# Kernel optimization log

Measured on AMD Instinct MI355X. Metric: run time of the kernel, lower is better.

## Reference

```python
import jax, jax.numpy as jnp
import numpy as np


def setup_inputs() -> dict:
    key = jax.random.key(0)
    k1, k2 = jax.random.split(key)
    B, H, W, D, K = 32, 64, 64, 64, 512
    x = jax.random.normal(k1, (B, H, W, D), dtype=jnp.float32)
    w = jax.random.normal(k2, (D, K), dtype=jnp.float32) * 0.05  # codebook (embedding_dim, num_embeddings)
    return {"x": x, "w": w}


def reference(x, w):
    commitment_cost = 1.0
    D = w.shape[0]
    z_e = x
    flat = x.reshape(-1, D)  # [N, D]
    # squared euclidean distances to each code: ||f||^2 - 2 f.w + ||w||^2 -> [N, K]
    distances = (jnp.sum(flat * flat, axis=1, keepdims=True)
                 - 2.0 * flat @ w
                 + jnp.sum(w * w, axis=0, keepdims=True))
    encoding_indices = jnp.argmax(-distances, axis=1).reshape(x.shape[:-1])  # [B,H,W]
    z_q = w.T[encoding_indices]  # embedding lookup -> [B,H,W,D]
    e_latent_loss = jnp.mean((jax.lax.stop_gradient(z_q) - z_e) ** 2)
    q_latent_loss = jnp.mean((z_q - jax.lax.stop_gradient(z_e)) ** 2)
    latent_loss = q_latent_loss + commitment_cost * e_latent_loss
    z_q_st = z_e + jax.lax.stop_gradient(z_q - z_e)  # straight-through estimator
    return encoding_indices, z_q_st, z_e, latent_loss
```

## Files before the change

kernel.cpp:

```cpp
#include <hip/hip_runtime.h>
#include <hip/hip_bf16.h>

#define NROWS   131072
#define DDIM    64
#define KCODES  512

#define RPB     128
#define NBLK    (NROWS / RPB)
#define CAP     16
#define THRESH  0.04f

#define WS_PART 0
#define WS_WT   2048
#define WS_WSQ  34816
#define WS_WTH  35328
#define WS_WTL  51712
#define WS_END  68096
#define WS_NEED_MFMA ((size_t)WS_END * sizeof(float))
#define WS_NEED_FALL ((size_t)35328 * sizeof(float))

#define NBLK_FB 1024

typedef __attribute__((ext_vector_type(8))) short short8;
typedef __attribute__((ext_vector_type(4))) float f32x4;

static __device__ __forceinline__ unsigned short f2bf(float v) {
  union { __hip_bfloat16 b; unsigned short u; } cv;
  cv.b = __float2bfloat16(v);
  return cv.u;
}
static __device__ __forceinline__ float bf2f(unsigned short u) {
  union { float f; unsigned v; } r;
  r.v = ((unsigned)u) << 16;
  return r.f;
}

static __device__ __forceinline__ float dot64(const float* __restrict__ xr,
                                              const float* __restrict__ wk) {
  const float4* __restrict__ w4 = (const float4*)wk;
  const float4* __restrict__ x4 = (const float4*)xr;
  float d = 0.f;
  {
    float4 wa0 = w4[0], wa1 = w4[1], wa2 = w4[2], wa3 = w4[3];
    float4 wa4 = w4[4], wa5 = w4[5], wa6 = w4[6], wa7 = w4[7];
    float4 xa0 = x4[0], xa1 = x4[1], xa2 = x4[2], xa3 = x4[3];
    float4 xa4 = x4[4], xa5 = x4[5], xa6 = x4[6], xa7 = x4[7];
    d = __builtin_fmaf(xa0.x, wa0.x, d); d = __builtin_fmaf(xa0.y, wa0.y, d);
    d = __builtin_fmaf(xa0.z, wa0.z, d); d = __builtin_fmaf(xa0.w, wa0.w, d);
    d = __builtin_fmaf(xa1.x, wa1.x, d); d = __builtin_fmaf(xa1.y, wa1.y, d);
    d = __builtin_fmaf(xa1.z, wa1.z, d); d = __builtin_fmaf(xa1.w, wa1.w, d);
    d = __builtin_fmaf(xa2.x, wa2.x, d); d = __builtin_fmaf(xa2.y, wa2.y, d);
    d = __builtin_fmaf(xa2.z, wa2.z, d); d = __builtin_fmaf(xa2.w, wa2.w, d);
    d = __builtin_fmaf(xa3.x, wa3.x, d); d = __builtin_fmaf(xa3.y, wa3.y, d);
    d = __builtin_fmaf(xa3.z, wa3.z, d); d = __builtin_fmaf(xa3.w, wa3.w, d);
    d = __builtin_fmaf(xa4.x, wa4.x, d); d = __builtin_fmaf(xa4.y, wa4.y, d);
    d = __builtin_fmaf(xa4.z, wa4.z, d); d = __builtin_fmaf(xa4.w, wa4.w, d);
    d = __builtin_fmaf(xa5.x, wa5.x, d); d = __builtin_fmaf(xa5.y, wa5.y, d);
    d = __builtin_fmaf(xa5.z, wa5.z, d); d = __builtin_fmaf(xa5.w, wa5.w, d);
    d = __builtin_fmaf(xa6.x, wa6.x, d); d = __builtin_fmaf(xa6.y, wa6.y, d);
    d = __builtin_fmaf(xa6.z, wa6.z, d); d = __builtin_fmaf(xa6.w, wa6.w, d);
    d = __builtin_fmaf(xa7.x, wa7.x, d); d = __builtin_fmaf(xa7.y, wa7.y, d);
    d = __builtin_fmaf(xa7.z, wa7.z, d); d = __builtin_fmaf(xa7.w, wa7.w, d);
  }
  {
    float4 wb0 = w4[8],  wb1 = w4[9],  wb2 = w4[10], wb3 = w4[11];
    float4 wb4 = w4[12], wb5 = w4[13], wb6 = w4[14], wb7 = w4[15];
    float4 xb0 = x4[8],  xb1 = x4[9],  xb2 = x4[10], xb3 = x4[11];
    float4 xb4 = x4[12], xb5 = x4[13], xb6 = x4[14], xb7 = x4[15];
    d = __builtin_fmaf(xb0.x, wb0.x, d); d = __builtin_fmaf(xb0.y, wb0.y, d);
    d = __builtin_fmaf(xb0.z, wb0.z, d); d = __builtin_fmaf(xb0.w, wb0.w, d);
    d = __builtin_fmaf(xb1.x, wb1.x, d); d = __builtin_fmaf(xb1.y, wb1.y, d);
    d = __builtin_fmaf(xb1.z, wb1.z, d); d = __builtin_fmaf(xb1.w, wb1.w, d);
    d = __builtin_fmaf(xb2.x, wb2.x, d); d = __builtin_fmaf(xb2.y, wb2.y, d);
    d = __builtin_fmaf(xb2.z, wb2.z, d); d = __builtin_fmaf(xb2.w, wb2.w, d);
    d = __builtin_fmaf(xb3.x, wb3.x, d); d = __builtin_fmaf(xb3.y, wb3.y, d);
    d = __builtin_fmaf(xb3.z, wb3.z, d); d = __builtin_fmaf(xb3.w, wb3.w, d);
    d = __builtin_fmaf(xb4.x, wb4.x, d); d = __builtin_fmaf(xb4.y, wb4.y, d);
    d = __builtin_fmaf(xb4.z, wb4.z, d); d = __builtin_fmaf(xb4.w, wb4.w, d);
    d = __builtin_fmaf(xb5.x, wb5.x, d); d = __builtin_fmaf(xb5.y, wb5.y, d);
    d = __builtin_fmaf(xb5.z, wb5.z, d); d = __builtin_fmaf(xb5.w, wb5.w, d);
    d = __builtin_fmaf(xb6.x, wb6.x, d); d = __builtin_fmaf(xb6.y, wb6.y, d);
    d = __builtin_fmaf(xb6.z, wb6.z, d); d = __builtin_fmaf(xb6.w, wb6.w, d);
    d = __builtin_fmaf(xb7.x, wb7.x, d); d = __builtin_fmaf(xb7.y, wb7.y, d);
    d = __builtin_fmaf(xb7.z, wb7.z, d); d = __builtin_fmaf(xb7.w, wb7.w, d);
  }
  return d;
}

__global__ void vq_prep_base(const float* __restrict__ w, float* __restrict__ wT,
                             float* __restrict__ wsq) {
  int g = blockIdx.x * 256 + threadIdx.x;
  wT[g] = w[(g & 63) * KCODES + (g >> 6)];
  if (g < KCODES) {
    float s = __fmul_rn(w[g], w[g]);
    for (int dd = 1; dd < DDIM; ++dd) {
      float v = w[dd * KCODES + g];
      s = __fadd_rn(s, __fmul_rn(v, v));
    }
    wsq[g] = s;
  }
}

__global__ void vq_prep_bf16(const float* __restrict__ wT,
                             unsigned short* __restrict__ wTh,
                             unsigned short* __restrict__ wTl) {
  int g = blockIdx.x * 256 + threadIdx.x;
  float v = wT[g];
  unsigned short h = f2bf(v);
  wTh[g] = h;
  wTl[g] = f2bf(v - bf2f(h));
}

__global__ __launch_bounds__(256) void vq_mfma(
    const float* __restrict__ x, const float* __restrict__ wT,
    const float* __restrict__ wsq, const unsigned short* __restrict__ wTh,
    const unsigned short* __restrict__ wTl, float* __restrict__ out_idx,
    float* __restrict__ out_zq, float* __restrict__ out_ze,
    float* __restrict__ lossPart) {
  __shared__ float xf[RPB * 68];
  __shared__ __attribute__((aligned(16))) char Bb[2][16384];
  __shared__ float wsq_s[KCODES];
  __shared__ float sumf_s[RPB];
  __shared__ int   idx_s[RPB];
  __shared__ int   cnt[RPB];
  __shared__ int   cand[RPB][CAP];
  __shared__ float loss_s[4];

  const int tid = threadIdx.x;
  const int wv = tid >> 6;
  const int lane = tid & 63;
  const int lr = lane & 15;
  const int kg = lane >> 4;
  const int rowBase = blockIdx.x * RPB;
  const float* xb = x + (size_t)rowBase * DDIM;

#pragma unroll
  for (int j = 0; j < 8; ++j) {
    int off = j * 1024 + tid * 4;
    float4 v = *(const float4*)(xb + off);
    int row = off >> 6, d0 = off & 63;
    *(float4*)&xf[row * 68 + d0] = v;
  }
  if (tid < 128) {
    cnt[tid] = 0;
    *(float4*)&wsq_s[tid * 4] = *(const float4*)&wsq[tid * 4];
  }

  const char* gH = (const char*)wTh;
  const char* gL = (const char*)wTl;
  float4 rH0, rH1, rL0, rL1;
#define LOADT(t)                                                   \
  {                                                                \
    const char* bh = gH + (size_t)(t) * 8192;                      \
    const char* bl = gL + (size_t)(t) * 8192;                      \
    rH0 = *(const float4*)(bh + tid * 16);                         \
    rH1 = *(const float4*)(bh + 4096 + tid * 16);                  \
    rL0 = *(const float4*)(bl + tid * 16);                         \
    rL1 = *(const float4*)(bl + 4096 + tid * 16);                  \
  }
  const int p0 = tid * 16, p1 = 4096 + tid * 16;
  const int cc0 = p0 >> 7, cc1 = p1 >> 7;
  const int w0 = cc0 * 128 + ((p0 & 127) ^ ((cc0 & 7) << 4));
  const int w1 = cc1 * 128 + ((p1 & 127) ^ ((cc1 & 7) << 4));
#define WRITET(buf)                                                \
  {                                                                \
    *(float4*)(Bb[buf] + w0) = rH0;                                \
    *(float4*)(Bb[buf] + w1) = rH1;                                \
    *(float4*)(Bb[buf] + 8192 + w0) = rL0;                         \
    *(float4*)(Bb[buf] + 8192 + w1) = rL1;                         \
  }

  LOADT(0);
  __syncthreads();

  short8 ah[2][2], al[2][2];
#pragma unroll
  for (int m = 0; m < 2; ++m)
#pragma unroll
    for (int kb = 0; kb < 2; ++kb) {
      const float* src = &xf[(wv * 32 + m * 16 + lr) * 68 + kb * 32 + kg * 8];
      short8 h, l;
#pragma unroll
      for (int j = 0; j < 8; ++j) {
        float v = src[j];
        unsigned short hu = f2bf(v);
        h[j] = (short)hu;
        l[j] = (short)f2bf(v - bf2f(hu));
      }
      ah[m][kb] = h;
      al[m][kb] = l;
    }

  if (lane < 32) {
    const float* xr = &xf[(wv * 32 + lane) * 68];
    float rr[8];
#pragma unroll
    for (int j = 0; j < 8; ++j) rr[j] = __fmul_rn(xr[j], xr[j]);
#pragma unroll
    for (int b = 1; b < 8; ++b)
#pragma unroll
      for (int j = 0; j < 8; ++j)
        rr[j] = __fadd_rn(rr[j], __fmul_rn(xr[b * 8 + j], xr[b * 8 + j]));
    float s01 = __fadd_rn(rr[0], rr[1]), s23 = __fadd_rn(rr[2], rr[3]);
    float s45 = __fadd_rn(rr[4], rr[5]), s67 = __fadd_rn(rr[6], rr[7]);
    sumf_s[wv * 32 + lane] = __fadd_rn(__fadd_rn(s01, s23), __fadd_rn(s45, s67));
  }

  WRITET(0);
  LOADT(1);
  __syncthreads();

  float rmin[2][4];
#pragma unroll
  for (int m = 0; m < 2; ++m)
#pragma unroll
    for (int q = 0; q < 4; ++q) rmin[m][q] = 3.4e38f;

  for (int t = 0; t < 8; ++t) {
    const char* bufc = Bb[t & 1];
    float sc[2][4][4];
#pragma unroll
    for (int n = 0; n < 4; ++n) {
      const int cc = n * 16 + lr;
      const int rowb = cc * 128;
      const int srow = (cc & 7) << 4;
      short8 bh0 = *(const short8*)(bufc + rowb + ((kg * 16) ^ srow));
      short8 bh1 = *(const short8*)(bufc + rowb + ((64 + kg * 16) ^ srow));
      short8 bl0 = *(const short8*)(bufc + 8192 + rowb + ((kg * 16) ^ srow));
      short8 bl1 = *(const short8*)(bufc + 8192 + rowb + ((64 + kg * 16) ^ srow));
      float wsqk = wsq_s[t * 64 + cc];
#pragma unroll
      for (int m = 0; m < 2; ++m) {
        f32x4 acc = {0.f, 0.f, 0.f, 0.f};
        acc = __builtin_amdgcn_mfma_f32_16x16x32_bf16(ah[m][0], bh0, acc, 0, 0, 0);
        acc = __builtin_amdgcn_mfma_f32_16x16x32_bf16(al[m][0], bh0, acc, 0, 0, 0);
        acc = __builtin_amdgcn_mfma_f32_16x16x32_bf16(ah[m][0], bl0, acc, 0, 0, 0);
        acc = __builtin_amdgcn_mfma_f32_16x16x32_bf16(ah[m][1], bh1, acc, 0, 0, 0);
        acc = __builtin_amdgcn_mfma_f32_16x16x32_bf16(al[m][1], bh1, acc, 0, 0, 0);
        acc = __builtin_amdgcn_mfma_f32_16x16x32_bf16(ah[m][1], bl1, acc, 0, 0, 0);
#pragma unroll
        for (int q = 0; q < 4; ++q)
          sc[m][n][q] = __builtin_fmaf(-2.0f, acc[q], wsqk);
      }
    }
#pragma unroll
    for (int m = 0; m < 2; ++m)
#pragma unroll
      for (int q = 0; q < 4; ++q) {
        float tm = fminf(fminf(sc[m][0][q], sc[m][1][q]),
                         fminf(sc[m][2][q], sc[m][3][q]));
#pragma unroll
        for (int s = 1; s < 16; s <<= 1) tm = fminf(tm, __shfl_xor(tm, s));
        float rm = fminf(rmin[m][q], tm);
        rmin[m][q] = rm;
        float thr = rm + THRESH;
        int rl = wv * 32 + m * 16 + kg * 4 + q;
#pragma unroll
        for (int n = 0; n < 4; ++n) {
          if (sc[m][n][q] <= thr) {
            int slot = atomicAdd(&cnt[rl], 1);
            if (slot < CAP) cand[rl][slot] = t * 64 + n * 16 + lr;
          }
        }
      }
    __syncthreads();
    if (t < 7) {
      WRITET((t + 1) & 1);
      if (t < 6) LOADT(t + 2);
      __syncthreads();
    }
  }

#pragma unroll 1
  for (int half = 0; half < 2; ++half) {
    const int myrow = wv * 32 + half * 16 + (lane >> 2);
    const int sub = lane & 3;
    const int cnr = cnt[myrow];
    const float* xr = &xf[myrow * 68];
    const float sf = sumf_s[myrow];
    float bd = 3.4e38f;
    int bk = 0x7fffffff;
    if (cnr <= CAP) {
#pragma unroll 1
      for (int s0 = 0; s0 < CAP; s0 += 4) {
        if (!__any(s0 + sub < cnr)) break;
        if (s0 + sub < cnr) {
          int k = cand[myrow][s0 + sub];
          float dot = dot64(xr, wT + k * DDIM);
          float dist = __fadd_rn(__fsub_rn(sf, __fmul_rn(2.0f, dot)), wsq[k]);
          if (dist < bd || (dist == bd && k < bk)) { bd = dist; bk = k; }
        }
      }
    } else {
      for (int k = sub; k < KCODES; k += 4) {
        float dot = dot64(xr, wT + k * DDIM);
        float dist = __fadd_rn(__fsub_rn(sf, __fmul_rn(2.0f, dot)), wsq[k]);
        if (dist < bd || (dist == bd && k < bk)) { bd = dist; bk = k; }
      }
    }
#pragma unroll
    for (int s = 1; s < 4; s <<= 1) {
      float od = __shfl_xor(bd, s);
      int ok = __shfl_xor(bk, s);
      if (od < bd || (od == bd && ok < bk)) { bd = od; bk = ok; }
    }
    if (sub == 0) idx_s[myrow] = bk;
  }

  float lsum = 0.f;
#pragma unroll
  for (int tt = 0; tt < 8; ++tt) {
    int row = wv * 32 + tt * 4 + (lane >> 4);
    int d0 = (lane & 15) * 4;
    int kf = idx_s[row];
    float4 xv = *(const float4*)&xf[row * 68 + d0];
    float4 wq = *(const float4*)&wT[kf * DDIM + d0];
    float4 zq;
    zq.x = __fadd_rn(xv.x, __fsub_rn(wq.x, xv.x));
    zq.y = __fadd_rn(xv.y, __fsub_rn(wq.y, xv.y));
    zq.z = __fadd_rn(xv.z, __fsub_rn(wq.z, xv.z));
    zq.w = __fadd_rn(xv.w, __fsub_rn(wq.w, xv.w));
    size_t go = (size_t)(rowBase + row) * DDIM + d0;
    *(float4*)(out_zq + go) = zq;
    *(float4*)(out_ze + go) = xv;
    float e0 = __fsub_rn(wq.x, xv.x), e1 = __fsub_rn(wq.y, xv.y);
    float e2 = __fsub_rn(wq.z, xv.z), e3 = __fsub_rn(wq.w, xv.w);
    lsum = __builtin_fmaf(e0, e0, lsum);
    lsum = __builtin_fmaf(e1, e1, lsum);
    lsum = __builtin_fmaf(e2, e2, lsum);
    lsum = __builtin_fmaf(e3, e3, lsum);
  }
#pragma unroll
  for (int s = 1; s < 64; s <<= 1) lsum += __shfl_xor(lsum, s);
  if (lane == 0) loss_s[wv] = lsum;
  if (lane < 32)
    out_idx[rowBase + wv * 32 + lane] = (float)idx_s[wv * 32 + lane];
  __syncthreads();
  if (tid == 0)
    lossPart[blockIdx.x] =
        __fadd_rn(__fadd_rn(__fadd_rn(loss_s[0], loss_s[1]), loss_s[2]), loss_s[3]);
}

template <int USE_WT, int LOSS_ATOMIC>
__global__ __launch_bounds__(256) void vq_fb(
    const float* __restrict__ x, const float* __restrict__ w,
    const float* __restrict__ wT,
    float* __restrict__ out_idx, float* __restrict__ out_zq,
    float* __restrict__ out_ze, float* __restrict__ lossOut) {
  __shared__ float xT[4][32 * 64];
  __shared__ float wtile[64 * 64];
  __shared__ float __attribute__((aligned(16))) sq_s[64];
  __shared__ float sumf_s[4][32];
  __shared__ int   idx_s[4][32];
  __shared__ float lsum_s[4];

  const int tid = threadIdx.x;
  const int wv = tid >> 6;
  const int lane = tid & 63;
  const int r = lane >> 3;
  const int c = lane & 7;
  const int rowBase = (blockIdx.x * 4 + wv) * 32;
  const float* xblk = x + (size_t)rowBase * DDIM;

#pragma unroll
  for (int j = 0; j < 8; ++j) {
    int off = j * 256 + lane * 4;
    float4 v = *(const float4*)(xblk + off);
    int row = off >> 6, d0 = off & 63;
    xT[wv][(d0 + 0) * 32 + row] = v.x;
    xT[wv][(d0 + 1) * 32 + row] = v.y;
    xT[wv][(d0 + 2) * 32 + row] = v.z;
    xT[wv][(d0 + 3) * 32 + row] = v.w;
  }
  __syncthreads();

  if (lane < 32) {
    float rr[8];
#pragma unroll
    for (int j = 0; j < 8; ++j) {
      float v = xT[wv][j * 32 + lane];
      rr[j] = __fmul_rn(v, v);
    }
#pragma unroll
    for (int blk = 1; blk < 8; ++blk)
#pragma unroll
      for (int j = 0; j < 8; ++j) {
        float v = xT[wv][(blk * 8 + j) * 32 + lane];
        rr[j] = __fadd_rn(rr[j], __fmul_rn(v, v));
      }
    float s01 = __fadd_rn(rr[0], rr[1]);
    float s23 = __fadd_rn(rr[2], rr[3]);
    float s45 = __fadd_rn(rr[4], rr[5]);
    float s67 = __fadd_rn(rr[6], rr[7]);
    sumf_s[wv][lane] = __fadd_rn(__fadd_rn(s01, s23), __fadd_rn(s45, s67));
  }

  float minv[4] = {3.4e38f, 3.4e38f, 3.4e38f, 3.4e38f};
  int mink[4] = {0, 0, 0, 0};

  for (int ct = 0; ct < 8; ++ct) {
#pragma unroll
    for (int j = 0; j < 4; ++j) {
      int off = j * 1024 + tid * 4;
      int d0 = off >> 6, kk = off & 63;
      *(float4*)&wtile[off] = *(const float4*)&w[d0 * KCODES + ct * 64 + kk];
    }
    __syncthreads();

    if (tid < 64) {
      float v0 = wtile[tid];
      float s = __fmul_rn(v0, v0);
      for (int d = 1; d < 64; ++d) {
        float v = wtile[d * 64 + tid];
        s = __fadd_rn(s, __fmul_rn(v, v));
      }
      sq_s[tid] = s;
    }

    float acc[4][8];
#pragma unroll
    for (int i = 0; i < 4; ++i)
#pragma unroll
      for (int j = 0; j < 8; ++j) acc[i][j] = 0.f;

#pragma unroll 4
    for (int d = 0; d < DDIM; ++d) {
      float4 a4 = *(const float4*)&xT[wv][d * 32 + r * 4];
      float4 b0 = *(const float4*)&wtile[d * 64 + c * 8];
      float4 b1 = *(const float4*)&wtile[d * 64 + c * 8 + 4];
      float a[4] = {a4.x, a4.y, a4.z, a4.w};
      float b[8] = {b0.x, b0.y, b0.z, b0.w, b1.x, b1.y, b1.z, b1.w};
#pragma unroll
      for (int i = 0; i < 4; ++i)
#pragma unroll
        for (int j = 0; j < 8; ++j)
          acc[i][j] = __builtin_fmaf(a[i], b[j], acc[i][j]);
    }
    __syncthreads();

#pragma unroll
    for (int i = 0; i < 4; ++i) {
      float sf = sumf_s[wv][r * 4 + i];
#pragma unroll
      for (int j = 0; j < 8; ++j) {
        float dist = __fadd_rn(__fsub_rn(sf, __fmul_rn(2.0f, acc[i][j])), sq_s[c * 8 + j]);
        int k = ct * 64 + c * 8 + j;
        if (dist < minv[i]) { minv[i] = dist; mink[i] = k; }
      }
    }
  }

#pragma unroll
  for (int i = 0; i < 4; ++i) {
    float v = minv[i];
    int kk = mink[i];
    for (int s = 1; s < 8; s <<= 1) {
      float ov = __shfl_xor(v, s);
      int ok = __shfl_xor(kk, s);
      if (ov < v || (ov == v && ok < kk)) { v = ov; kk = ok; }
    }
    if (c == 0) idx_s[wv][r * 4 + i] = kk;
  }

  float lsum = 0.f;
  for (int rowi = 0; rowi < 32; ++rowi) {
    int k = idx_s[wv][rowi];
    size_t go = (size_t)(rowBase + rowi) * DDIM + lane;
    float xv = xblk[rowi * DDIM + lane];
    float wvv = USE_WT ? wT[k * DDIM + lane] : w[lane * KCODES + k];
    out_zq[go] = __fadd_rn(xv, __fsub_rn(wvv, xv));
    out_ze[go] = xv;
    float dd = __fsub_rn(wvv, xv);
    lsum = __builtin_fmaf(dd, dd, lsum);
  }
#pragma unroll
  for (int s = 1; s < 64; s <<= 1) lsum += __shfl_xor(lsum, s);
  if (lane == 0) lsum_s[wv] = lsum;
  __syncthreads();
  if (tid == 0) {
    float part = __fadd_rn(__fadd_rn(__fadd_rn(lsum_s[0], lsum_s[1]), lsum_s[2]), lsum_s[3]);
    if (LOSS_ATOMIC) atomicAdd(lossOut, part);
    else lossOut[blockIdx.x] = part;
  }
  if (lane < 32)
    out_idx[rowBase + lane] = (float)idx_s[wv][lane];
}

__global__ void vq_loss(const float* __restrict__ part, int npart,
                        float* __restrict__ out_loss) {
  float s = 0.f;
  for (int i = threadIdx.x; i < npart; i += 64) s += part[i];
#pragma unroll
  for (int t = 1; t < 64; t <<= 1) s += __shfl_xor(s, t);
  if (threadIdx.x == 0) out_loss[0] = s * (1.0f / 4194304.0f);
}

extern "C" void kernel_launch(void* const* d_in, const int* in_sizes, int n_in,
                              void* d_out, int out_size, void* d_ws, size_t ws_size,
                              hipStream_t stream) {
  const float* x = (const float*)d_in[0];
  const float* w = (const float*)d_in[1];
  float* ob = (float*)d_out;
  float* out_idx = ob;
  float* out_zq = ob + NROWS;
  float* out_ze = out_zq + (size_t)NROWS * DDIM;
  float* out_loss = out_ze + (size_t)NROWS * DDIM;
  float* wsf = (float*)d_ws;

  if (ws_size >= WS_NEED_MFMA) {
    vq_prep_base<<<128, 256, 0, stream>>>(w, wsf + WS_WT, wsf + WS_WSQ);
    vq_prep_bf16<<<128, 256, 0, stream>>>(wsf + WS_WT,
                                          (unsigned short*)(wsf + WS_WTH),
                                          (unsigned short*)(wsf + WS_WTL));
    vq_mfma<<<NBLK, 256, 0, stream>>>(x, wsf + WS_WT, wsf + WS_WSQ,
                                      (const unsigned short*)(wsf + WS_WTH),
                                      (const unsigned short*)(wsf + WS_WTL),
                                      out_idx, out_zq, out_ze, wsf + WS_PART);
    vq_loss<<<1, 64, 0, stream>>>(wsf + WS_PART, NBLK, out_loss);
  } else if (ws_size >= WS_NEED_FALL) {
    vq_prep_base<<<128, 256, 0, stream>>>(w, wsf + WS_WT, wsf + WS_WSQ);
    vq_fb<1, 0><<<NBLK_FB, 256, 0, stream>>>(x, w, wsf + WS_WT, out_idx,
                                             out_zq, out_ze, wsf + WS_PART);
    vq_loss<<<1, 64, 0, stream>>>(wsf + WS_PART, NBLK_FB, out_loss);
  } else {
    hipMemsetAsync(out_loss, 0, sizeof(float), stream);
    vq_fb<0, 1><<<NBLK_FB, 256, 0, stream>>>(x, w, nullptr, out_idx,
                                             out_zq, out_ze, out_loss);
    vq_loss<<<1, 64, 0, stream>>>(out_loss, 1, out_loss);
  }
}
```

Before: 97.03 us.

## Drop LDS staging of x and wsq, halve candidate cap, raise occupancy

```diff
diff --git a/kernel.cpp b/kernel.cpp
--- a/kernel.cpp
+++ b/kernel.cpp
@@ -7,7 +7,7 @@
 
 #define RPB     128
 #define NBLK    (NROWS / RPB)
-#define CAP     16
+#define CAP     8
 #define THRESH  0.04f
 
 #define WS_PART 0
@@ -111,15 +111,13 @@
   wTl[g] = f2bf(v - bf2f(h));
 }
 
-__global__ __launch_bounds__(256) void vq_mfma(
+__global__ __launch_bounds__(256, 4) void vq_mfma(
     const float* __restrict__ x, const float* __restrict__ wT,
     const float* __restrict__ wsq, const unsigned short* __restrict__ wTh,
     const unsigned short* __restrict__ wTl, float* __restrict__ out_idx,
     float* __restrict__ out_zq, float* __restrict__ out_ze,
     float* __restrict__ lossPart) {
-  __shared__ float xf[RPB * 68];
   __shared__ __attribute__((aligned(16))) char Bb[2][16384];
-  __shared__ float wsq_s[KCODES];
   __shared__ float sumf_s[RPB];
   __shared__ int   idx_s[RPB];
   __shared__ int   cnt[RPB];
@@ -133,18 +131,6 @@
   const int kg = lane >> 4;
   const int rowBase = blockIdx.x * RPB;
   const float* xb = x + (size_t)rowBase * DDIM;
-
-#pragma unroll
-  for (int j = 0; j < 8; ++j) {
-    int off = j * 1024 + tid * 4;
-    float4 v = *(const float4*)(xb + off);
-    int row = off >> 6, d0 = off & 63;
-    *(float4*)&xf[row * 68 + d0] = v;
-  }
-  if (tid < 128) {
-    cnt[tid] = 0;
-    *(float4*)&wsq_s[tid * 4] = *(const float4*)&wsq[tid * 4];
-  }
 
   const char* gH = (const char*)wTh;
   const char* gL = (const char*)wTl;
@@ -171,28 +157,30 @@
   }
 
   LOADT(0);
-  __syncthreads();
+  if (tid < RPB) cnt[tid] = 0;
 
   short8 ah[2][2], al[2][2];
 #pragma unroll
   for (int m = 0; m < 2; ++m)
 #pragma unroll
     for (int kb = 0; kb < 2; ++kb) {
-      const float* src = &xf[(wv * 32 + m * 16 + lr) * 68 + kb * 32 + kg * 8];
+      const float* src = xb + (size_t)(wv * 32 + m * 16 + lr) * DDIM + kb * 32 + kg * 8;
+      float4 v0 = *(const float4*)src;
+      float4 v1 = *(const float4*)(src + 4);
+      float vv[8] = {v0.x, v0.y, v0.z, v0.w, v1.x, v1.y, v1.z, v1.w};
       short8 h, l;
 #pragma unroll
       for (int j = 0; j < 8; ++j) {
-        float v = src[j];
-        unsigned short hu = f2bf(v);
+        unsigned short hu = f2bf(vv[j]);
         h[j] = (short)hu;
-        l[j] = (short)f2bf(v - bf2f(hu));
+        l[j] = (short)f2bf(vv[j] - bf2f(hu));
       }
       ah[m][kb] = h;
       al[m][kb] = l;
     }
 
-  if (lane < 32) {
-    const float* xr = &xf[(wv * 32 + lane) * 68];
+  if (tid < RPB) {
+    const float* xr = xb + (size_t)tid * DDIM;
     float rr[8];
 #pragma unroll
     for (int j = 0; j < 8; ++j) rr[j] = __fmul_rn(xr[j], xr[j]);
@@ -203,7 +191,7 @@
         rr[j] = __fadd_rn(rr[j], __fmul_rn(xr[b * 8 + j], xr[b * 8 + j]));
     float s01 = __fadd_rn(rr[0], rr[1]), s23 = __fadd_rn(rr[2], rr[3]);
     float s45 = __fadd_rn(rr[4], rr[5]), s67 = __fadd_rn(rr[6], rr[7]);
-    sumf_s[wv * 32 + lane] = __fadd_rn(__fadd_rn(s01, s23), __fadd_rn(s45, s67));
+    sumf_s[tid] = __fadd_rn(__fadd_rn(s01, s23), __fadd_rn(s45, s67));
   }
 
   WRITET(0);
@@ -228,7 +216,7 @@
       short8 bh1 = *(const short8*)(bufc + rowb + ((64 + kg * 16) ^ srow));
       short8 bl0 = *(const short8*)(bufc + 8192 + rowb + ((kg * 16) ^ srow));
       short8 bl1 = *(const short8*)(bufc + 8192 + rowb + ((64 + kg * 16) ^ srow));
-      float wsqk = wsq_s[t * 64 + cc];
+      float wsqk = wsq[t * 64 + cc];
 #pragma unroll
       for (int m = 0; m < 2; ++m) {
         f32x4 acc = {0.f, 0.f, 0.f, 0.f};
@@ -263,7 +251,6 @@
           }
         }
       }
-    __syncthreads();
     if (t < 7) {
       WRITET((t + 1) & 1);
       if (t < 6) LOADT(t + 2);
@@ -276,7 +263,7 @@
     const int myrow = wv * 32 + half * 16 + (lane >> 2);
     const int sub = lane & 3;
     const int cnr = cnt[myrow];
-    const float* xr = &xf[myrow * 68];
+    const float* xr = xb + (size_t)myrow * DDIM;
     const float sf = sumf_s[myrow];
     float bd = 3.4e38f;
     int bk = 0x7fffffff;
@@ -313,7 +300,7 @@
     int row = wv * 32 + tt * 4 + (lane >> 4);
     int d0 = (lane & 15) * 4;
     int kf = idx_s[row];
-    float4 xv = *(const float4*)&xf[row * 68 + d0];
+    float4 xv = *(const float4*)(xb + (size_t)row * DDIM + d0);
     float4 wq = *(const float4*)&wT[kf * DDIM + d0];
     float4 zq;
     zq.x = __fadd_rn(xv.x, __fsub_rn(wq.x, xv.x));
```

New measurement: 206.3 us. 113% more time.

## Halve rows per block, shrink candidate cap, and read code norms from global

Applied to the files above, without the earlier changes.

```diff
diff --git a/kernel.cpp b/kernel.cpp
--- a/kernel.cpp
+++ b/kernel.cpp
@@ -5,9 +5,9 @@
 #define DDIM    64
 #define KCODES  512
 
-#define RPB     128
+#define RPB     64
 #define NBLK    (NROWS / RPB)
-#define CAP     16
+#define CAP     8
 #define THRESH  0.04f
 
 #define WS_PART 0
@@ -111,7 +111,7 @@
   wTl[g] = f2bf(v - bf2f(h));
 }
 
-__global__ __launch_bounds__(256) void vq_mfma(
+__global__ __launch_bounds__(256, 3) void vq_mfma(
     const float* __restrict__ x, const float* __restrict__ wT,
     const float* __restrict__ wsq, const unsigned short* __restrict__ wTh,
     const unsigned short* __restrict__ wTl, float* __restrict__ out_idx,
@@ -119,7 +119,6 @@
     float* __restrict__ lossPart) {
   __shared__ float xf[RPB * 68];
   __shared__ __attribute__((aligned(16))) char Bb[2][16384];
-  __shared__ float wsq_s[KCODES];
   __shared__ float sumf_s[RPB];
   __shared__ int   idx_s[RPB];
   __shared__ int   cnt[RPB];
@@ -135,16 +134,13 @@
   const float* xb = x + (size_t)rowBase * DDIM;
 
 #pragma unroll
-  for (int j = 0; j < 8; ++j) {
+  for (int j = 0; j < 4; ++j) {
     int off = j * 1024 + tid * 4;
     float4 v = *(const float4*)(xb + off);
     int row = off >> 6, d0 = off & 63;
     *(float4*)&xf[row * 68 + d0] = v;
   }
-  if (tid < 128) {
-    cnt[tid] = 0;
-    *(float4*)&wsq_s[tid * 4] = *(const float4*)&wsq[tid * 4];
-  }
+  if (tid < RPB) cnt[tid] = 0;
 
   const char* gH = (const char*)wTh;
   const char* gL = (const char*)wTl;
@@ -173,26 +169,24 @@
   LOADT(0);
   __syncthreads();
 
-  short8 ah[2][2], al[2][2];
-#pragma unroll
-  for (int m = 0; m < 2; ++m)
-#pragma unroll
-    for (int kb = 0; kb < 2; ++kb) {
-      const float* src = &xf[(wv * 32 + m * 16 + lr) * 68 + kb * 32 + kg * 8];
-      short8 h, l;
-#pragma unroll
-      for (int j = 0; j < 8; ++j) {
-        float v = src[j];
-        unsigned short hu = f2bf(v);
-        h[j] = (short)hu;
-        l[j] = (short)f2bf(v - bf2f(hu));
-      }
-      ah[m][kb] = h;
-      al[m][kb] = l;
-    }
-
-  if (lane < 32) {
-    const float* xr = &xf[(wv * 32 + lane) * 68];
+  short8 ah[2], al[2];
+#pragma unroll
+  for (int kb = 0; kb < 2; ++kb) {
+    const float* src = &xf[(wv * 16 + lr) * 68 + kb * 32 + kg * 8];
+    short8 h, l;
+#pragma unroll
+    for (int j = 0; j < 8; ++j) {
+      float v = src[j];
+      unsigned short hu = f2bf(v);
+      h[j] = (short)hu;
+      l[j] = (short)f2bf(v - bf2f(hu));
+    }
+    ah[kb] = h;
+    al[kb] = l;
+  }
+
+  if (tid < RPB) {
+    const float* xr = &xf[tid * 68];
     float rr[8];
 #pragma unroll
     for (int j = 0; j < 8; ++j) rr[j] = __fmul_rn(xr[j], xr[j]);
@@ -203,22 +197,18 @@
         rr[j] = __fadd_rn(rr[j], __fmul_rn(xr[b * 8 + j], xr[b * 8 + j]));
     float s01 = __fadd_rn(rr[0], rr[1]), s23 = __fadd_rn(rr[2], rr[3]);
     float s45 = __fadd_rn(rr[4], rr[5]), s67 = __fadd_rn(rr[6], rr[7]);
-    sumf_s[wv * 32 + lane] = __fadd_rn(__fadd_rn(s01, s23), __fadd_rn(s45, s67));
+    sumf_s[tid] = __fadd_rn(__fadd_rn(s01, s23), __fadd_rn(s45, s67));
   }
 
   WRITET(0);
   LOADT(1);
   __syncthreads();
 
-  float rmin[2][4];
-#pragma unroll
-  for (int m = 0; m < 2; ++m)
-#pragma unroll
-    for (int q = 0; q < 4; ++q) rmin[m][q] = 3.4e38f;
+  float rmin[4] = {3.4e38f, 3.4e38f, 3.4e38f, 3.4e38f};
 
   for (int t = 0; t < 8; ++t) {
     const char* bufc = Bb[t & 1];
-    float sc[2][4][4];
+    float sc[4][4];
 #pragma unroll
     for (int n = 0; n < 4; ++n) {
       const int cc = n * 16 + lr;
@@ -228,41 +218,35 @@
       short8 bh1 = *(const short8*)(bufc + rowb + ((64 + kg * 16) ^ srow));
       short8 bl0 = *(const short8*)(bufc + 8192 + rowb + ((kg * 16) ^ srow));
       short8 bl1 = *(const short8*)(bufc + 8192 + rowb + ((64 + kg * 16) ^ srow));
-      float wsqk = wsq_s[t * 64 + cc];
-#pragma unroll
-      for (int m = 0; m < 2; ++m) {
-        f32x4 acc = {0.f, 0.f, 0.f, 0.f};
-        acc = __builtin_amdgcn_mfma_f32_16x16x32_bf16(ah[m][0], bh0, acc, 0, 0, 0);
-        acc = __builtin_amdgcn_mfma_f32_16x16x32_bf16(al[m][0], bh0, acc, 0, 0, 0);
-        acc = __builtin_amdgcn_mfma_f32_16x16x32_bf16(ah[m][0], bl0, acc, 0, 0, 0);
-        acc = __builtin_amdgcn_mfma_f32_16x16x32_bf16(ah[m][1], bh1, acc, 0, 0, 0);
-        acc = __builtin_amdgcn_mfma_f32_16x16x32_bf16(al[m][1], bh1, acc, 0, 0, 0);
-        acc = __builtin_amdgcn_mfma_f32_16x16x32_bf16(ah[m][1], bl1, acc, 0, 0, 0);
-#pragma unroll
-        for (int q = 0; q < 4; ++q)
-          sc[m][n][q] = __builtin_fmaf(-2.0f, acc[q], wsqk);
-      }
-    }
-#pragma unroll
-    for (int m = 0; m < 2; ++m)
-#pragma unroll
-      for (int q = 0; q < 4; ++q) {
-        float tm = fminf(fminf(sc[m][0][q], sc[m][1][q]),
-                         fminf(sc[m][2][q], sc[m][3][q]));
-#pragma unroll
-        for (int s = 1; s < 16; s <<= 1) tm = fminf(tm, __shfl_xor(tm, s));
-        float rm = fminf(rmin[m][q], tm);
-        rmin[m][q] = rm;
-        float thr = rm + THRESH;
-        int rl = wv * 32 + m * 16 + kg * 4 + q;
-#pragma unroll
-        for (int n = 0; n < 4; ++n) {
-          if (sc[m][n][q] <= thr) {
-            int slot = atomicAdd(&cnt[rl], 1);
-            if (slot < CAP) cand[rl][slot] = t * 64 + n * 16 + lr;
-          }
+      float wsqk = wsq[t * 64 + cc];
+      f32x4 acc = {0.f, 0.f, 0.f, 0.f};
+      acc = __builtin_amdgcn_mfma_f32_16x16x32_bf16(ah[0], bh0, acc, 0, 0, 0);
+      acc = __builtin_amdgcn_mfma_f32_16x16x32_bf16(al[0], bh0, acc, 0, 0, 0);
+      acc = __builtin_amdgcn_mfma_f32_16x16x32_bf16(ah[0], bl0, acc, 0, 0, 0);
+      acc = __builtin_amdgcn_mfma_f32_16x16x32_bf16(ah[1], bh1, acc, 0, 0, 0);
+      acc = __builtin_amdgcn_mfma_f32_16x16x32_bf16(al[1], bh1, acc, 0, 0, 0);
+      acc = __builtin_amdgcn_mfma_f32_16x16x32_bf16(ah[1], bl1, acc, 0, 0, 0);
+#pragma unroll
+      for (int q = 0; q < 4; ++q)
+        sc[n][q] = __builtin_fmaf(-2.0f, acc[q], wsqk);
+    }
+#pragma unroll
+    for (int q = 0; q < 4; ++q) {
+      float tm = fminf(fminf(sc[0][q], sc[1][q]), fminf(sc[2][q], sc[3][q]));
+#pragma unroll
+      for (int s = 1; s < 16; s <<= 1) tm = fminf(tm, __shfl_xor(tm, s));
+      float rm = fminf(rmin[q], tm);
+      rmin[q] = rm;
+      float thr = rm + THRESH;
+      int rl = wv * 16 + kg * 4 + q;
+#pragma unroll
+      for (int n = 0; n < 4; ++n) {
+        if (sc[n][q] <= thr) {
+          int slot = atomicAdd(&cnt[rl], 1);
+          if (slot < CAP) cand[rl][slot] = t * 64 + n * 16 + lr;
         }
       }
+    }
     __syncthreads();
     if (t < 7) {
       WRITET((t + 1) & 1);
@@ -271,9 +255,8 @@
     }
   }
 
-#pragma unroll 1
-  for (int half = 0; half < 2; ++half) {
-    const int myrow = wv * 32 + half * 16 + (lane >> 2);
+  {
+    const int myrow = wv * 16 + (lane >> 2);
     const int sub = lane & 3;
     const int cnr = cnt[myrow];
     const float* xr = &xf[myrow * 68];
@@ -309,8 +292,8 @@
 
   float lsum = 0.f;
 #pragma unroll
-  for (int tt = 0; tt < 8; ++tt) {
-    int row = wv * 32 + tt * 4 + (lane >> 4);
+  for (int tt = 0; tt < 4; ++tt) {
+    int row = wv * 16 + tt * 4 + (lane >> 4);
     int d0 = (lane & 15) * 4;
     int kf = idx_s[row];
     float4 xv = *(const float4*)&xf[row * 68 + d0];
@@ -333,8 +316,8 @@
 #pragma unroll
   for (int s = 1; s < 64; s <<= 1) lsum += __shfl_xor(lsum, s);
   if (lane == 0) loss_s[wv] = lsum;
-  if (lane < 32)
-    out_idx[rowBase + wv * 32 + lane] = (float)idx_s[wv * 32 + lane];
+  if (lane < 16)
+    out_idx[rowBase + wv * 16 + lane] = (float)idx_s[wv * 16 + lane];
   __syncthreads();
   if (tid == 0)
     lossPart[blockIdx.x] =
```

Measured after the change: 148.4 us. +52.9%, slower.
